# Optimization experiments

Hardware: AMD Instinct MI355X
Metric: run time of the kernel (lower is better)

The kernel has to match this reference:

```python
import jax, jax.numpy as jnp
import numpy as np

RY = jnp.array([[-1.0, 0.0, 0.0], [0.0, 1.0, 0.0], [0.0, 0.0, -1.0]], dtype=jnp.float32)


def quat2mat(q):
    # q: [N,4] -> [N,3,3], same formula as the torch quaternion2matrix (no normalization)
    q0, q1, q2, q3 = q[:, 0], q[:, 1], q[:, 2], q[:, 3]
    r0 = jnp.stack([q0*q0 + q1*q1 - q2*q2 - q3*q3, 2*(q1*q2 - q0*q3), 2*(q1*q3 + q0*q2)], axis=-1)
    r1 = jnp.stack([2*(q1*q2 + q0*q3), q0*q0 - q1*q1 + q2*q2 - q3*q3, 2*(q2*q3 - q0*q1)], axis=-1)
    r2 = jnp.stack([2*(q1*q3 - q0*q2), 2*(q2*q3 + q0*q1), q0*q0 - q1*q1 - q2*q2 + q3*q3], axis=-1)
    return jnp.stack([r0, r1, r2], axis=-2)


def setup_inputs() -> dict:
    key = jax.random.key(0)
    k1, k2, k3, k4, k5, k6 = jax.random.split(key, 6)
    B, H, W, N = 256, 256, 256, 8192
    return {
        "confidence": jax.random.normal(k1, (B, 1, H, W), dtype=jnp.float32),
        "confidence_gt": jax.random.normal(k2, (B, 1, H, W), dtype=jnp.float32),
        "weight": jax.random.uniform(k3, (B, H, W), dtype=jnp.float32),
        "depth_and_rotation": jax.random.normal(k4, (N, 5), dtype=jnp.float32),
        "ann_values": jax.random.normal(k5, (N, 5), dtype=jnp.float32),
        "ann_flags": jax.random.randint(k6, (N,), 0, 2).astype(bool),
    }


def reference(confidence, confidence_gt, weight, depth_and_rotation, ann_values, ann_flags):
    # confidence loss
    diff = confidence[:, 0, ...] - confidence_gt[:, 0, ...]
    confidence_loss = jnp.sum(weight * diff * diff) / (256.0 * 256.0)

    N = ann_values.shape[0]
    mask = ann_flags.astype(jnp.float32)  # [N]

    # depth loss
    d_err = (depth_and_rotation[:, 0] - ann_values[:, 0]) ** 2
    depth_loss = jnp.sum(mask * d_err) / N

    # rotation loss: gt matrix from raw quaternion (unnormalized, as in original),
    # pred matrix from normalized predicted quaternion
    m_pred = quat2mat(ann_values[:, 1:])                      # [N,3,3]
    q = depth_and_rotation[:, 1:]
    q = q / jnp.linalg.norm(q, axis=-1, keepdims=True)
    m_gt = quat2mat(q)                                        # [N,3,3]
    n1 = jnp.linalg.norm((m_gt - m_pred).reshape(N, 9), axis=-1)
    m_pred_ry = jnp.einsum('nij,jk->nik', m_pred, RY)
    n2 = jnp.linalg.norm((m_gt - m_pred_ry).reshape(N, 9), axis=-1)
    rotation_loss = jnp.sum(mask * jnp.minimum(n1, n2)) / N

    return (confidence_loss, depth_loss, rotation_loss)
```

## Files before the change

### kernel.cpp

```cpp
#include <hip/hip_runtime.h>

#define NBLOCKS 1024
#define NTHREADS 256

__device__ __forceinline__ float wave_reduce_sum(float v) {
#pragma unroll
    for (int off = 32; off > 0; off >>= 1)
        v += __shfl_down(v, off, 64);
    return v;
}

__device__ __forceinline__ void quat2mat(float q0, float q1, float q2, float q3,
                                         float m[9]) {
    float q00 = q0 * q0, q11 = q1 * q1, q22 = q2 * q2, q33 = q3 * q3;
    m[0] = q00 + q11 - q22 - q33;
    m[1] = 2.0f * (q1 * q2 - q0 * q3);
    m[2] = 2.0f * (q1 * q3 + q0 * q2);
    m[3] = 2.0f * (q1 * q2 + q0 * q3);
    m[4] = q00 - q11 + q22 - q33;
    m[5] = 2.0f * (q2 * q3 - q0 * q1);
    m[6] = 2.0f * (q1 * q3 - q0 * q2);
    m[7] = 2.0f * (q2 * q3 + q0 * q1);
    m[8] = q00 - q11 - q22 + q33;
}

__global__ __launch_bounds__(NTHREADS) void hpnet_loss_kernel(
    const float* __restrict__ conf,
    const float* __restrict__ conf_gt,
    const float* __restrict__ weight,
    const float* __restrict__ dr,
    const float* __restrict__ ann,
    const int*   __restrict__ flags,
    float* __restrict__ out,
    long long n_conf, int N) {
    const long long gid = (long long)blockIdx.x * blockDim.x + threadIdx.x;
    const long long gstride = (long long)gridDim.x * blockDim.x;

    const float4* __restrict__ c4 = (const float4*)conf;
    const float4* __restrict__ g4 = (const float4*)conf_gt;
    const float4* __restrict__ w4 = (const float4*)weight;
    const long long n4 = n_conf >> 2;

    float acc_c = 0.0f;
    for (long long i = gid; i < n4; i += gstride) {
        float4 c = c4[i];
        float4 g = g4[i];
        float4 w = w4[i];
        float d0 = c.x - g.x, d1 = c.y - g.y, d2 = c.z - g.z, d3 = c.w - g.w;
        acc_c += w.x * d0 * d0 + w.y * d1 * d1 + w.z * d2 * d2 + w.w * d3 * d3;
    }

    float acc_d = 0.0f;
    float acc_r = 0.0f;
    for (long long n = gid; n < N; n += gstride) {
        float m = flags[n] ? 1.0f : 0.0f;

        float de = dr[n * 5 + 0] - ann[n * 5 + 0];
        acc_d += m * de * de;

        float mp[9];
        quat2mat(ann[n * 5 + 1], ann[n * 5 + 2], ann[n * 5 + 3], ann[n * 5 + 4], mp);

        float p0 = dr[n * 5 + 1], p1 = dr[n * 5 + 2], p2 = dr[n * 5 + 3],
              p3 = dr[n * 5 + 4];
        float inv = 1.0f / sqrtf(p0 * p0 + p1 * p1 + p2 * p2 + p3 * p3);
        float mg[9];
        quat2mat(p0 * inv, p1 * inv, p2 * inv, p3 * inv, mg);

        float s1 = 0.0f, s2 = 0.0f;
#pragma unroll
        for (int r = 0; r < 3; ++r) {
            float a0 = mg[r * 3 + 0], a1 = mg[r * 3 + 1], a2 = mg[r * 3 + 2];
            float b0 = mp[r * 3 + 0], b1 = mp[r * 3 + 1], b2 = mp[r * 3 + 2];
            float e0 = a0 - b0, e1 = a1 - b1, e2 = a2 - b2;
            s1 += e0 * e0 + e1 * e1 + e2 * e2;
            float f0 = a0 + b0, f2 = a2 + b2;
            s2 += f0 * f0 + e1 * e1 + f2 * f2;
        }
        acc_r += m * fminf(sqrtf(s1), sqrtf(s2));
    }

    acc_c = wave_reduce_sum(acc_c);
    acc_d = wave_reduce_sum(acc_d);
    acc_r = wave_reduce_sum(acc_r);

    __shared__ float s_c[NTHREADS / 64], s_d[NTHREADS / 64], s_r[NTHREADS / 64];
    const int lane = threadIdx.x & 63;
    const int wid = threadIdx.x >> 6;
    if (lane == 0) {
        s_c[wid] = acc_c;
        s_d[wid] = acc_d;
        s_r[wid] = acc_r;
    }
    __syncthreads();
    if (threadIdx.x == 0) {
        float tc = 0.0f, td = 0.0f, tr = 0.0f;
#pragma unroll
        for (int w = 0; w < NTHREADS / 64; ++w) {
            tc += s_c[w];
            td += s_d[w];
            tr += s_r[w];
        }
        atomicAdd(&out[0], tc * (1.0f / (256.0f * 256.0f)));
        atomicAdd(&out[1], td * (1.0f / 8192.0f));
        atomicAdd(&out[2], tr * (1.0f / 8192.0f));
    }
}

extern "C" void kernel_launch(void* const* d_in, const int* in_sizes, int n_in,
                              void* d_out, int out_size, void* d_ws,
                              size_t ws_size, hipStream_t stream) {
    const float* conf    = (const float*)d_in[0];
    const float* conf_gt = (const float*)d_in[1];
    const float* weight  = (const float*)d_in[2];
    const float* dr      = (const float*)d_in[3];
    const float* ann     = (const float*)d_in[4];
    const int*   flags   = (const int*)d_in[5];
    float* out = (float*)d_out;

    const long long n_conf = (long long)in_sizes[0];
    const int N = in_sizes[5];

    hipMemsetAsync(d_out, 0, 3 * sizeof(float), stream);

    hpnet_loss_kernel<<<NBLOCKS, NTHREADS, 0, stream>>>(
        conf, conf_gt, weight, dr, ann, flags, out, n_conf, N);
}
```

Measured before the change: 223.7 us.

## Replace atomics with two-pass reduction, double grid, unroll streaming loop by two

Doubles the grid size and unrolls the grid-stride confidence loop by two, so each thread has two sets of float4 loads in flight. The memset and global float atomics are replaced by per-block partials written to workspace and summed in a second single-block kernel. The goal is more memory-level parallelism on a bandwidth-bound stream of about 200MB, at the cost of an extra kernel launch.

```diff
diff --git a/kernel.cpp b/kernel.cpp
--- a/kernel.cpp
+++ b/kernel.cpp
@@ -1,6 +1,6 @@
 #include <hip/hip_runtime.h>
 
-#define NBLOCKS 1024
+#define NBLOCKS 2048
 #define NTHREADS 256
 
 __device__ __forceinline__ float wave_reduce_sum(float v) {
@@ -24,14 +24,39 @@
     m[8] = q00 - q11 - q22 + q33;
 }
 
-__global__ __launch_bounds__(NTHREADS) void hpnet_loss_kernel(
-    const float* __restrict__ conf,
-    const float* __restrict__ conf_gt,
-    const float* __restrict__ weight,
-    const float* __restrict__ dr,
-    const float* __restrict__ ann,
-    const int*   __restrict__ flags,
-    float* __restrict__ out,
+__device__ __forceinline__ void block_reduce3(float c, float d, float r,
+                                              float* dst) {
+    c = wave_reduce_sum(c);
+    d = wave_reduce_sum(d);
+    r = wave_reduce_sum(r);
+    __shared__ float s_c[NTHREADS / 64], s_d[NTHREADS / 64], s_r[NTHREADS / 64];
+    const int lane = threadIdx.x & 63;
+    const int wid = threadIdx.x >> 6;
+    if (lane == 0) {
+        s_c[wid] = c;
+        s_d[wid] = d;
+        s_r[wid] = r;
+    }
+    __syncthreads();
+    if (threadIdx.x == 0) {
+        float tc = 0.0f, td = 0.0f, tr = 0.0f;
+#pragma unroll
+        for (int w = 0; w < NTHREADS / 64; ++w) {
+            tc += s_c[w];
+            td += s_d[w];
+            tr += s_r[w];
+        }
+        dst[0] = tc;
+        dst[1] = td;
+        dst[2] = tr;
+    }
+}
+
+__global__ __launch_bounds__(NTHREADS) void hpnet_partial_kernel(
+    const float* __restrict__ conf, const float* __restrict__ conf_gt,
+    const float* __restrict__ weight, const float* __restrict__ dr,
+    const float* __restrict__ ann, const int* __restrict__ flags,
+    float* __restrict__ part,
     long long n_conf, int N) {
     const long long gid = (long long)blockIdx.x * blockDim.x + threadIdx.x;
     const long long gstride = (long long)gridDim.x * blockDim.x;
@@ -41,14 +66,27 @@
     const float4* __restrict__ w4 = (const float4*)weight;
     const long long n4 = n_conf >> 2;
 
-    float acc_c = 0.0f;
-    for (long long i = gid; i < n4; i += gstride) {
-        float4 c = c4[i];
-        float4 g = g4[i];
-        float4 w = w4[i];
-        float d0 = c.x - g.x, d1 = c.y - g.y, d2 = c.z - g.z, d3 = c.w - g.w;
-        acc_c += w.x * d0 * d0 + w.y * d1 * d1 + w.z * d2 * d2 + w.w * d3 * d3;
+    float acc_a = 0.0f, acc_b = 0.0f;
+    for (long long i = gid; i < n4; i += 2 * gstride) {
+        float4 c0 = c4[i];
+        float4 g0 = g4[i];
+        float4 w0 = w4[i];
+        long long j = i + gstride;
+        if (j < n4) {
+            float4 c1 = c4[j];
+            float4 g1 = g4[j];
+            float4 w1 = w4[j];
+            float d0 = c1.x - g1.x, d1 = c1.y - g1.y, d2 = c1.z - g1.z,
+                  d3 = c1.w - g1.w;
+            acc_b += w1.x * d0 * d0 + w1.y * d1 * d1 + w1.z * d2 * d2 +
+                     w1.w * d3 * d3;
+        }
+        float d0 = c0.x - g0.x, d1 = c0.y - g0.y, d2 = c0.z - g0.z,
+              d3 = c0.w - g0.w;
+        acc_a += w0.x * d0 * d0 + w0.y * d1 * d1 + w0.z * d2 * d2 +
+                 w0.w * d3 * d3;
     }
+    float acc_c = acc_a + acc_b;
 
     float acc_d = 0.0f;
     float acc_r = 0.0f;
@@ -59,7 +97,8 @@
         acc_d += m * de * de;
 
         float mp[9];
-        quat2mat(ann[n * 5 + 1], ann[n * 5 + 2], ann[n * 5 + 3], ann[n * 5 + 4], mp);
+        quat2mat(ann[n * 5 + 1], ann[n * 5 + 2], ann[n * 5 + 3],
+                 ann[n * 5 + 4], mp);
 
         float p0 = dr[n * 5 + 1], p1 = dr[n * 5 + 2], p2 = dr[n * 5 + 3],
               p3 = dr[n * 5 + 4];
@@ -80,30 +119,25 @@
         acc_r += m * fminf(sqrtf(s1), sqrtf(s2));
     }
 
-    acc_c = wave_reduce_sum(acc_c);
-    acc_d = wave_reduce_sum(acc_d);
-    acc_r = wave_reduce_sum(acc_r);
+    block_reduce3(acc_c, acc_d, acc_r, &part[3 * blockIdx.x]);
+}
 
-    __shared__ float s_c[NTHREADS / 64], s_d[NTHREADS / 64], s_r[NTHREADS / 64];
-    const int lane = threadIdx.x & 63;
-    const int wid = threadIdx.x >> 6;
-    if (lane == 0) {
-        s_c[wid] = acc_c;
-        s_d[wid] = acc_d;
-        s_r[wid] = acc_r;
+__global__ __launch_bounds__(NTHREADS) void hpnet_final_kernel(
+    const float* __restrict__ part,
+    float* __restrict__ out) {
+    float tc = 0.0f, td = 0.0f, tr = 0.0f;
+    for (int i = threadIdx.x; i < NBLOCKS; i += NTHREADS) {
+        tc += part[3 * i + 0];
+        td += part[3 * i + 1];
+        tr += part[3 * i + 2];
     }
+    __shared__ float dst[3];
+    block_reduce3(tc, td, tr, dst);
     __syncthreads();
     if (threadIdx.x == 0) {
-        float tc = 0.0f, td = 0.0f, tr = 0.0f;
-#pragma unroll
-        for (int w = 0; w < NTHREADS / 64; ++w) {
-            tc += s_c[w];
-            td += s_d[w];
-            tr += s_r[w];
-        }
-        atomicAdd(&out[0], tc * (1.0f / (256.0f * 256.0f)));
-        atomicAdd(&out[1], td * (1.0f / 8192.0f));
-        atomicAdd(&out[2], tr * (1.0f / 8192.0f));
+        out[0] = dst[0] * (1.0f / (256.0f * 256.0f));
+        out[1] = dst[1] * (1.0f / 8192.0f);
+        out[2] = dst[2] * (1.0f / 8192.0f);
     }
 }
 
@@ -117,12 +151,12 @@
     const float* ann     = (const float*)d_in[4];
     const int*   flags   = (const int*)d_in[5];
     float* out = (float*)d_out;
+    float* part = (float*)d_ws;
 
     const long long n_conf = (long long)in_sizes[0];
     const int N = in_sizes[5];
 
-    hipMemsetAsync(d_out, 0, 3 * sizeof(float), stream);
-
-    hpnet_loss_kernel<<<NBLOCKS, NTHREADS, 0, stream>>>(
-        conf, conf_gt, weight, dr, ann, flags, out, n_conf, N);
+    hpnet_partial_kernel<<<NBLOCKS, NTHREADS, 0, stream>>>(
+        conf, conf_gt, weight, dr, ann, flags, part, n_conf, N);
+    hpnet_final_kernel<<<1, NTHREADS, 0, stream>>>(part, out);
 }
```

After: 203.5 us. 1.1x faster.
